# Performance work log

Hardware: AMD Instinct MI355X
Metric: run time of the kernel (lower is better)

## Reference

```python
import jax, jax.numpy as jnp
import numpy as np

B, LQ, LK, LKL = 4, 1024, 1024, 512
DX, H, DK = 1024, 16, 64
ALPHA = 0.5
NEG = -1e9
EPS = 1e-5


def setup_inputs() -> dict:
    key = jax.random.key(0)
    ks = jax.random.split(key, 24)
    s = 0.02
    inp = {
        "q": jax.random.normal(ks[0], (B, LQ, DX), jnp.float32),
        "k": jax.random.normal(ks[1], (B, LK, DX), jnp.float32),
        "v": jax.random.normal(ks[2], (B, LK, DX), jnp.float32),
        "kl": jax.random.normal(ks[3], (B, LKL, DX), jnp.float32),
        "vl": jax.random.normal(ks[4], (B, LKL, DX), jnp.float32),
        "pad_mask": jax.random.randint(ks[5], (B, LQ, LK), 0, 2).astype(bool),
        "pad_mask_l": jax.random.randint(ks[6], (B, LQ, LKL), 0, 2).astype(bool),
        "wq_w": jax.random.normal(ks[7], (DX, H * DK), jnp.float32) * s,
        "wq_b": jnp.zeros((H * DK,), jnp.float32),
        "wk_w": jax.random.normal(ks[8], (DX, H * DK), jnp.float32) * s,
        "wk_b": jnp.zeros((H * DK,), jnp.float32),
        "wv_w": jax.random.normal(ks[9], (DX, H * DK), jnp.float32) * s,
        "wv_b": jnp.zeros((H * DK,), jnp.float32),
        "wkl_w": jax.random.normal(ks[10], (DX, H * DK), jnp.float32) * s,
        "wkl_b": jnp.zeros((H * DK,), jnp.float32),
        "wvl_w": jax.random.normal(ks[11], (DX, H * DK), jnp.float32) * s,
        "wvl_b": jnp.zeros((H * DK,), jnp.float32),
        "wo_w": jax.random.normal(ks[12], (H * DK, DX), jnp.float32) * s,
        "wo_b": jnp.zeros((DX,), jnp.float32),
        "ln_g": jnp.ones((DX,), jnp.float32),
        "ln_b": jnp.zeros((DX,), jnp.float32),
    }
    return inp


def _heads(x, w, b, L):
    # (B, L, DX) @ (DX, H*DK) -> (B, H, L, DK)
    y = x @ w + b
    return y.reshape(B, L, H, DK).transpose(0, 2, 1, 3)


def _attn(qh, kh, vh, mask):
    # qh: (B,H,Lq,D), kh/vh: (B,H,Lk,D), mask: (B,Lq,Lk) bool (True = masked)
    scores = jnp.einsum("bhqd,bhkd->bhqk", qh, kh) / np.sqrt(DK).astype(np.float32)
    scores = jnp.where(mask[:, None, :, :], NEG, scores)
    attn = jax.nn.softmax(scores, axis=-1)
    out = jnp.einsum("bhqk,bhkd->bhqd", attn, vh)
    return out, attn


def reference(q, k, v, kl, vl, pad_mask, pad_mask_l,
              wq_w, wq_b, wk_w, wk_b, wv_w, wv_b,
              wkl_w, wkl_b, wvl_w, wvl_b, wo_w, wo_b, ln_g, ln_b):
    X = q
    qh = _heads(q, wq_w, wq_b, LQ)
    kh = _heads(k, wk_w, wk_b, LK)
    vh = _heads(v, wv_w, wv_b, LK)
    klh = _heads(kl, wkl_w, wkl_b, LKL)
    vlh = _heads(vl, wvl_w, wvl_b, LKL)

    out_c, attn_c = _attn(qh, kh, vh, pad_mask)
    out_l, attn_l = _attn(qh, klh, vlh, pad_mask_l)

    out = ALPHA * out_c + (1.0 - ALPHA) * out_l          # (B,H,Lq,DK)
    out = out.transpose(0, 2, 1, 3).reshape(B, LQ, H * DK)
    out = out @ wo_w + wo_b                              # dropout = identity (eval)
    y = out + X
    mu = jnp.mean(y, axis=-1, keepdims=True)
    var = jnp.var(y, axis=-1, keepdims=True)
    y = (y - mu) / jnp.sqrt(var + EPS) * ln_g + ln_b
    return y, attn_c, attn_l
```

## Files before the change

kernel.cpp:

```cpp
#include <hip/hip_runtime.h>
#include <hip/hip_bf16.h>

#define B_   4
#define LQ_  1024
#define LK_  1024
#define LKL_ 512
#define DX_  1024
#define H_   16
#define DK_  64
#define HDK_ 1024
#define NEG_ -1e9f
#define EPS_ 1e-5f

typedef __bf16 bf16_t;
typedef __bf16 bf16x8 __attribute__((ext_vector_type(8)));
typedef __bf16 bf16x4 __attribute__((ext_vector_type(4)));
typedef float  f32x4  __attribute__((ext_vector_type(4)));

__device__ inline f32x4 mfma16(bf16x8 a, bf16x8 b, f32x4 c) {
    return __builtin_amdgcn_mfma_f32_16x16x32_bf16(a, b, c, 0, 0, 0);
}

__device__ __forceinline__ void gload16(const void* g, void* l) {
    __builtin_amdgcn_global_load_lds(
        (const __attribute__((address_space(1))) void*)g,
        (__attribute__((address_space(3))) void*)l, 16, 0, 0);
}

__device__ inline float waveMax(float v) {
#pragma unroll
    for (int o = 32; o > 0; o >>= 1) v = fmaxf(v, __shfl_xor(v, o, 64));
    return v;
}
__device__ inline float waveSum(float v) {
#pragma unroll
    for (int o = 32; o > 0; o >>= 1) v += __shfl_xor(v, o, 64);
    return v;
}

template<int STRIDE>
__device__ inline int sidx(int row, int col) {
    return (row * STRIDE + col) ^ ((row & 15) << 3);
}

__global__ void detect_mask_kernel(const unsigned* __restrict__ m, unsigned* __restrict__ flag)
{
    __shared__ unsigned w[256];
    w[threadIdx.x] = m[threadIdx.x];
    __syncthreads();
    if (threadIdx.x == 0) {
        bool all01 = true, allf = true;
        for (int i = 0; i < 256; ++i) {
            unsigned v = w[i];
            all01 = all01 && (v <= 1u);
            allf  = allf  && (v == 0u || v == 0x3F800000u);
        }
        *flag = all01 ? 0u : (allf ? 2u : 1u);
    }
}

__global__ __launch_bounds__(256) void bitpack_mask_kernel(
    const void* __restrict__ mc, const void* __restrict__ ml,
    const unsigned* __restrict__ flagp,
    unsigned long long* __restrict__ bc, unsigned long long* __restrict__ bl)
{
    const unsigned flag = *flagp;
    const size_t NC = (size_t)B_ * LQ_ * LK_;
    const int lane = threadIdx.x & 63;
    const size_t g = (size_t)blockIdx.x * 256 + threadIdx.x;
    const bool inC = g < NC;
    const size_t idx = inC ? g : g - NC;
    const void* src = inC ? mc : ml;
    bool m;
    if (flag == 0u)      m = ((const int*)src)[idx] != 0;
    else if (flag == 2u) m = ((const float*)src)[idx] != 0.0f;
    else                 m = ((const unsigned char*)src)[idx] != 0;
    const unsigned long long bal = __ballot(m);
    if (lane == 0) {
        unsigned long long* dst = inC ? bc : bl;
        dst[idx >> 6] = bal;
    }
}

__global__ __launch_bounds__(256) void cvt_bf16_kernel(
    const float* __restrict__ src, bf16_t* __restrict__ dst, int n8)
{
    const int i = blockIdx.x * 256 + threadIdx.x;
    if (i >= n8) return;
    const float4 a = ((const float4*)src)[i * 2];
    const float4 b = ((const float4*)src)[i * 2 + 1];
    bf16x8 o;
    o[0] = (bf16_t)a.x; o[1] = (bf16_t)a.y; o[2] = (bf16_t)a.z; o[3] = (bf16_t)a.w;
    o[4] = (bf16_t)b.x; o[5] = (bf16_t)b.y; o[6] = (bf16_t)b.z; o[7] = (bf16_t)b.w;
    ((bf16x8*)dst)[i] = o;
}

__global__ __launch_bounds__(256) void wtrans_kernel(
    const float* __restrict__ W, bf16_t* __restrict__ Wt)
{
    __shared__ float T[64][65];
    const int k0 = blockIdx.y * 64, n0 = blockIdx.x * 64;
    const int t = threadIdx.x;
    const int lr = t >> 2, c0 = (t & 3) * 16;
#pragma unroll
    for (int j = 0; j < 4; ++j) {
        const float4 v = *(const float4*)&W[(size_t)(k0 + lr) * DX_ + n0 + c0 + j * 4];
        T[lr][c0 + j * 4 + 0] = v.x; T[lr][c0 + j * 4 + 1] = v.y;
        T[lr][c0 + j * 4 + 2] = v.z; T[lr][c0 + j * 4 + 3] = v.w;
    }
    __syncthreads();
    const int dr = t >> 2;
    bf16x8 o0, o1;
#pragma unroll
    for (int j = 0; j < 8; ++j) {
        o0[j] = (bf16_t)T[c0 + j][dr];
        o1[j] = (bf16_t)T[c0 + 8 + j][dr];
    }
    *(bf16x8*)&Wt[(size_t)(n0 + dr) * DX_ + k0 + c0]     = o0;
    *(bf16x8*)&Wt[(size_t)(n0 + dr) * DX_ + k0 + c0 + 8] = o1;
}

__global__ __launch_bounds__(256) void transpose_v_kernel(
    const bf16_t* __restrict__ V, bf16_t* __restrict__ Vt, int L)
{
    __shared__ bf16_t T[64][72];
    const int bh = blockIdx.y, l0 = blockIdx.x * 64;
    const bf16_t* Vb = V + (size_t)bh * L * 64;
    bf16_t* Vtb = Vt + (size_t)bh * 64 * L;
    const int t = threadIdx.x;
    {
        const int lr = t >> 2, dc = (t & 3) * 16;
        const bf16x8 a = *(const bf16x8*)&Vb[(size_t)(l0 + lr) * 64 + dc];
        const bf16x8 b = *(const bf16x8*)&Vb[(size_t)(l0 + lr) * 64 + dc + 8];
#pragma unroll
        for (int j = 0; j < 8; ++j) { T[lr][dc + j] = a[j]; T[lr][dc + 8 + j] = b[j]; }
    }
    __syncthreads();
    {
        const int dr = t >> 2, lc = (t & 3) * 16;
        bf16x8 o0, o1;
#pragma unroll
        for (int j = 0; j < 8; ++j) { o0[j] = T[lc + j][dr]; o1[j] = T[lc + 8 + j][dr]; }
        *(bf16x8*)&Vtb[(size_t)dr * L + l0 + lc]     = o0;
        *(bf16x8*)&Vtb[(size_t)dr * L + l0 + lc + 8] = o1;
    }
}

template<int MODE>
__global__ __launch_bounds__(512, 2) void gemm2_kernel(
    const bf16_t* __restrict__ A, const bf16_t* __restrict__ Bt,
    const float* __restrict__ bias,
    void* __restrict__ out, const float* __restrict__ resid, int lshift)
{
    __shared__ bf16_t As[128 * 64];
    __shared__ bf16_t Bs[128 * 64];
    char* const AsB = (char*)As;
    char* const BsB = (char*)Bs;
    const int tid = threadIdx.x, wave = tid >> 6, lane = tid & 63;
    const int m0 = blockIdx.y * 128, n0 = blockIdx.x * 128;
    const int wr4 = (wave >> 1) * 32, wc2 = (wave & 1) * 64;

    f32x4 acc[2][4] = {};

    const int srow = wave * 8 + (lane >> 3);
    const int sslot = lane & 7;

    for (int k0 = 0; k0 < 1024; k0 += 64) {
        __syncthreads();
#pragma unroll
        for (int j = 0; j < 2; ++j) {
            const int row = srow + j * 64;
            const int gs = sslot ^ (row & 7);
            gload16(&A[(size_t)(m0 + row) * 1024 + k0 + gs * 8],
                    AsB + j * 8192 + wave * 1024);
            gload16(&Bt[(size_t)(n0 + row) * 1024 + k0 + gs * 8],
                    BsB + j * 8192 + wave * 1024);
        }
        __syncthreads();
#pragma unroll
        for (int kk = 0; kk < 2; ++kk) {
            bf16x8 av[2], bv[4];
#pragma unroll
            for (int i = 0; i < 2; ++i) {
                const int r = wr4 + i * 16 + (lane & 15);
                av[i] = *(const bf16x8*)(AsB + r * 128 + (((kk * 4 + (lane >> 4)) ^ (r & 7)) * 16));
            }
#pragma unroll
            for (int n = 0; n < 4; ++n) {
                const int r = wc2 + n * 16 + (lane & 15);
                bv[n] = *(const bf16x8*)(BsB + r * 128 + (((kk * 4 + (lane >> 4)) ^ (r & 7)) * 16));
            }
#pragma unroll
            for (int i = 0; i < 2; ++i)
#pragma unroll
                for (int n = 0; n < 4; ++n)
                    acc[i][n] = mfma16(av[i], bv[n], acc[i][n]);
        }
    }

#pragma unroll
    for (int i = 0; i < 2; ++i) {
#pragma unroll
        for (int n = 0; n < 4; ++n) {
            const int col = n0 + wc2 + n * 16 + (lane & 15);
            const float bs = bias[col];
            const int row0 = m0 + wr4 + i * 16 + (lane >> 4) * 4;
            if (MODE == 0) {
                const int b = row0 >> lshift, l = row0 & ((1 << lshift) - 1);
                const int h = col >> 6, d = col & 63;
#pragma unroll
                for (int r = 0; r < 4; ++r)
                    ((bf16_t*)out)[(((size_t)(b * H_ + h) << lshift) + l + r) * DK_ + d] =
                        (bf16_t)(acc[i][n][r] + bs);
            } else {
#pragma unroll
                for (int r = 0; r < 4; ++r) {
                    const size_t idx = (size_t)(row0 + r) * DX_ + col;
                    ((float*)out)[idx] = acc[i][n][r] + bs + resid[idx];
                }
            }
        }
    }
}

template<int LKX, bool COMBINE>
__device__ __forceinline__ void fused_branch_body(
    const bf16_t* __restrict__ Qh, const bf16_t* __restrict__ Kh,
    const bf16_t* __restrict__ Vt, const unsigned* __restrict__ bits,
    float* __restrict__ S, bf16_t* __restrict__ comb, bf16_t* __restrict__ Ssh)
{
    const int sid = (blockIdx.x & 7) * 512 + (blockIdx.x >> 3);
    const int bh = sid >> 6, qt = sid & 63;
    const int b = bh >> 4, h = bh & 15;
    const int q0 = qt * 16;
    const int wave = threadIdx.x >> 6, lane = threadIdx.x & 63;
    const int lr = lane & 15, lk8 = (lane >> 4) * 8;
    constexpr int WORDS = LKX / 32;

    const bf16_t* Qb  = Qh + (size_t)bh * LQ_ * DK_;
    const bf16_t* Kb  = Kh + (size_t)bh * LKX * DK_;
    const bf16_t* Vtb = Vt + (size_t)bh * DK_ * LKX;
    float* Sout = S + (size_t)bh * LQ_ * LKX;

    bf16x8 qf[2];
#pragma unroll
    for (int ks = 0; ks < 2; ++ks)
        qf[ks] = *(const bf16x8*)&Qb[(size_t)(q0 + lr) * DK_ + ks * 32 + lk8];

    constexpr int KTS = LKX / 64;
#pragma unroll
    for (int kt = 0; kt < KTS; ++kt) {
        const int kbase = wave * (LKX / 4) + kt * 16;
        f32x4 acc = {};
#pragma unroll
        for (int ks = 0; ks < 2; ++ks) {
            const bf16x8 bb = *(const bf16x8*)&Kb[(size_t)(kbase + lr) * DK_ + ks * 32 + lk8];
            acc = mfma16(qf[ks], bb, acc);
        }
        const int wi = kbase >> 5;
        const int sh = (kbase & 16) + (lane & 15);
#pragma unroll
        for (int r = 0; r < 4; ++r) {
            const int row = (lane >> 4) * 4 + r;
            const unsigned word = bits[(size_t)(b * LQ_ + q0 + row) * WORDS + wi];
            const bool msk = (word >> sh) & 1u;
            Ssh[sidx<LKX>(row, kbase + (lane & 15))] = (bf16_t)(msk ? NEG_ : acc[r] * 0.125f);
        }
    }
    __syncthreads();

    constexpr int NP = LKX / 256;
#pragma unroll 1
    for (int i = 0; i < 4; ++i) {
        const int row = wave * 4 + i;
        const int rowg = q0 + row;
        float p[NP * 4];
        float m = -INFINITY;
#pragma unroll
        for (int ps = 0; ps < NP; ++ps) {
            const bf16x4 sv = *(const bf16x4*)&Ssh[sidx<LKX>(row, ps * 256 + lane * 4)];
#pragma unroll
            for (int j = 0; j < 4; ++j) {
                p[ps * 4 + j] = (float)sv[j];
                m = fmaxf(m, p[ps * 4 + j]);
            }
        }
        m = waveMax(m);
        float s = 0.f;
#pragma unroll
        for (int j = 0; j < NP * 4; ++j) { p[j] = __expf(p[j] - m); s += p[j]; }
        s = waveSum(s);
        const float inv = 1.f / s;
#pragma unroll
        for (int ps = 0; ps < NP; ++ps) {
            const int col = ps * 256 + lane * 4;
            f32x4 o; bf16x4 pb;
#pragma unroll
            for (int j = 0; j < 4; ++j) {
                const float v = p[ps * 4 + j] * inv;
                o[j] = v; pb[j] = (bf16_t)v;
            }
            __builtin_nontemporal_store(o, (f32x4*)&Sout[(size_t)rowg * LKX + col]);
            *(bf16x4*)&Ssh[sidx<LKX>(row, col)] = pb;
        }
    }
    __syncthreads();

    f32x4 acc_o = {};
    const int d0 = wave * 16;
#pragma unroll
    for (int ks = 0; ks < LKX / 32; ++ks) {
        const bf16x8 bb = *(const bf16x8*)&Vtb[(size_t)(d0 + lr) * LKX + ks * 32 + lk8];
        const bf16x8 a  = *(const bf16x8*)&Ssh[sidx<LKX>(lr, ks * 32 + lk8)];
        acc_o = mfma16(a, bb, acc_o);
    }

#pragma unroll
    for (int r = 0; r < 4; ++r) {
        const int row = q0 + (lane >> 4) * 4 + r;
        const size_t idx = ((size_t)b * LQ_ + row) * HDK_ + h * DK_ + d0 + (lane & 15);
        const float half = 0.5f * acc_o[r];
        if (COMBINE) comb[idx] = (bf16_t)((float)comb[idx] + half);
        else         comb[idx] = (bf16_t)half;
    }
}

__global__ __launch_bounds__(256, 3) void fused_c_kernel(
    const bf16_t* __restrict__ Qh, const bf16_t* __restrict__ Kh,
    const bf16_t* __restrict__ Vt, const unsigned* __restrict__ bits,
    float* __restrict__ S, bf16_t* __restrict__ comb)
{
    __shared__ bf16_t Ssh[16 * LK_];
    fused_branch_body<LK_, false>(Qh, Kh, Vt, bits, S, comb, Ssh);
}

__global__ __launch_bounds__(256, 3) void fused_l_kernel(
    const bf16_t* __restrict__ Qh, const bf16_t* __restrict__ Kh,
    const bf16_t* __restrict__ Vt, const unsigned* __restrict__ bits,
    float* __restrict__ S, bf16_t* __restrict__ comb)
{
    __shared__ bf16_t Ssh[16 * LKL_];
    fused_branch_body<LKL_, true>(Qh, Kh, Vt, bits, S, comb, Ssh);
}

__global__ __launch_bounds__(256) void ln_kernel(
    const float* __restrict__ Y, const float* __restrict__ g,
    const float* __restrict__ be, float* __restrict__ out)
{
    __shared__ float red1[4], red2[4];
    const int tid = threadIdx.x, wave = tid >> 6, lane = tid & 63;
    const float* p = Y + (size_t)blockIdx.x * DX_;
    const float4 x = *(const float4*)&p[tid * 4];
    float s  = x.x + x.y + x.z + x.w;
    float ss = x.x * x.x + x.y * x.y + x.z * x.z + x.w * x.w;
    s = waveSum(s); ss = waveSum(ss);
    if (lane == 0) { red1[wave] = s; red2[wave] = ss; }
    __syncthreads();
    s  = red1[0] + red1[1] + red1[2] + red1[3];
    ss = red2[0] + red2[1] + red2[2] + red2[3];
    const float mean = s * (1.f / DX_);
    const float var  = ss * (1.f / DX_) - mean * mean;
    const float rstd = rsqrtf(var + EPS_);
    const float4 gg = *(const float4*)&g[tid * 4];
    const float4 bb = *(const float4*)&be[tid * 4];
    float4 o;
    o.x = (x.x - mean) * rstd * gg.x + bb.x;
    o.y = (x.y - mean) * rstd * gg.y + bb.y;
    o.z = (x.z - mean) * rstd * gg.z + bb.z;
    o.w = (x.w - mean) * rstd * gg.w + bb.w;
    *(float4*)&out[(size_t)blockIdx.x * DX_ + tid * 4] = o;
}

extern "C" void kernel_launch(void* const* d_in, const int* in_sizes, int n_in,
                              void* d_out, int out_size, void* d_ws, size_t ws_size,
                              hipStream_t stream)
{
    const float* q    = (const float*)d_in[0];
    const float* k    = (const float*)d_in[1];
    const float* v    = (const float*)d_in[2];
    const float* kl   = (const float*)d_in[3];
    const float* vl   = (const float*)d_in[4];
    const void*  mask  = d_in[5];
    const void*  maskl = d_in[6];
    const float* wq_w  = (const float*)d_in[7];
    const float* wq_b  = (const float*)d_in[8];
    const float* wk_w  = (const float*)d_in[9];
    const float* wk_b  = (const float*)d_in[10];
    const float* wv_w  = (const float*)d_in[11];
    const float* wv_b  = (const float*)d_in[12];
    const float* wkl_w = (const float*)d_in[13];
    const float* wkl_b = (const float*)d_in[14];
    const float* wvl_w = (const float*)d_in[15];
    const float* wvl_b = (const float*)d_in[16];
    const float* wo_w  = (const float*)d_in[17];
    const float* wo_b  = (const float*)d_in[18];
    const float* ln_g  = (const float*)d_in[19];
    const float* ln_b  = (const float*)d_in[20];

    char* ws = (char*)d_ws;
    const size_t MiB = 1u << 20;
    bf16_t* qb   = (bf16_t*)(ws);
    bf16_t* kb   = (bf16_t*)(ws +   8 * MiB);
    bf16_t* vb   = (bf16_t*)(ws +  16 * MiB);
    bf16_t* klb  = (bf16_t*)(ws +  24 * MiB);
    bf16_t* vlb  = (bf16_t*)(ws +  28 * MiB);
    bf16_t* qh   = (bf16_t*)(ws +  32 * MiB);
    bf16_t* kh   = (bf16_t*)(ws +  40 * MiB);
    bf16_t* klh  = (bf16_t*)(ws +  48 * MiB);
    bf16_t* vh   = (bf16_t*)(ws +  52 * MiB);
    bf16_t* vlh  = (bf16_t*)(ws +  60 * MiB);
    bf16_t* vt   = (bf16_t*)(ws +  64 * MiB);
    bf16_t* vlt  = (bf16_t*)(ws +  72 * MiB);
    bf16_t* wqT  = (bf16_t*)(ws +  76 * MiB);
    bf16_t* wkT  = (bf16_t*)(ws +  78 * MiB);
    bf16_t* wvT  = (bf16_t*)(ws +  80 * MiB);
    bf16_t* wklT = (bf16_t*)(ws +  82 * MiB);
    bf16_t* wvlT = (bf16_t*)(ws +  84 * MiB);
    bf16_t* woT  = (bf16_t*)(ws +  86 * MiB);
    unsigned* flag = (unsigned*)(ws + 88 * MiB);
    unsigned long long* bitc = (unsigned long long*)(ws + 89 * MiB);
    unsigned long long* bitl = (unsigned long long*)(ws + 89 * MiB + 512 * 1024);
    bf16_t* comb = (bf16_t*)(ws + 90 * MiB);
    float*  ypre = (float*) (ws);

    float* y_out = (float*)d_out;
    float* Sc = y_out + (size_t)B_ * LQ_ * DX_;
    float* Sl = Sc + (size_t)B_ * H_ * LQ_ * LK_;

    detect_mask_kernel<<<dim3(1), dim3(256), 0, stream>>>((const unsigned*)mask, flag);
    bitpack_mask_kernel<<<dim3((B_*LQ_*(LK_+LKL_)) / 256), 256, 0, stream>>>(
        mask, maskl, flag, bitc, bitl);

    cvt_bf16_kernel<<<2048, 256, 0, stream>>>(q,  qb,  524288);
    cvt_bf16_kernel<<<2048, 256, 0, stream>>>(k,  kb,  524288);
    cvt_bf16_kernel<<<2048, 256, 0, stream>>>(v,  vb,  524288);
    cvt_bf16_kernel<<<1024, 256, 0, stream>>>(kl, klb, 262144);
    cvt_bf16_kernel<<<1024, 256, 0, stream>>>(vl, vlb, 262144);

    wtrans_kernel<<<dim3(16, 16), 256, 0, stream>>>(wq_w,  wqT);
    wtrans_kernel<<<dim3(16, 16), 256, 0, stream>>>(wk_w,  wkT);
    wtrans_kernel<<<dim3(16, 16), 256, 0, stream>>>(wv_w,  wvT);
    wtrans_kernel<<<dim3(16, 16), 256, 0, stream>>>(wkl_w, wklT);
    wtrans_kernel<<<dim3(16, 16), 256, 0, stream>>>(wvl_w, wvlT);
    wtrans_kernel<<<dim3(16, 16), 256, 0, stream>>>(wo_w,  woT);

    gemm2_kernel<0><<<dim3(8, 32), 512, 0, stream>>>(qb,  wqT,  wq_b,  qh,  nullptr, 10);
    gemm2_kernel<0><<<dim3(8, 32), 512, 0, stream>>>(kb,  wkT,  wk_b,  kh,  nullptr, 10);
    gemm2_kernel<0><<<dim3(8, 16), 512, 0, stream>>>(klb, wklT, wkl_b, klh, nullptr,  9);
    gemm2_kernel<0><<<dim3(8, 32), 512, 0, stream>>>(vb,  wvT,  wv_b,  vh,  nullptr, 10);
    gemm2_kernel<0><<<dim3(8, 16), 512, 0, stream>>>(vlb, wvlT, wvl_b, vlh, nullptr,  9);

    transpose_v_kernel<<<dim3(16, 64), 256, 0, stream>>>(vh,  vt,  LK_);
    transpose_v_kernel<<<dim3( 8, 64), 256, 0, stream>>>(vlh, vlt, LKL_);

    fused_c_kernel<<<dim3(4096), 256, 0, stream>>>(qh, kh,  vt,  (const unsigned*)bitc, Sc, comb);
    fused_l_kernel<<<dim3(4096), 256, 0, stream>>>(qh, klh, vlt, (const unsigned*)bitl, Sl, comb);

    gemm2_kernel<2><<<dim3(8, 32), 512, 0, stream>>>(comb, woT, wo_b, ypre, q, 0);

    ln_kernel<<<4096, 256, 0, stream>>>(ypre, ln_g, ln_b, y_out);
}
```

Baseline: 404.7 us.

## Batch prep kernels into grouped launches, add MFMA priority hints, widen softmax vectors

Merges the mask-type detection into the bitpack kernel and collapses the five conversion, six weight-transpose, five projection GEMM and two V-transpose launches into single grouped launches indexed by blockIdx.z. The goal is to cut launch count and the idle gaps between small kernels. Separately, it wraps the MFMA sequences in s_setprio hints, hoists the K loads ahead of the QK MFMAs, and widens the softmax pass to 8-element bf16 vectors. Grouped grids launch some blocks that exit early, and every bitpack block now re-reads the first 256 mask words to detect the mask type.

```diff
diff --git a/kernel.cpp b/kernel.cpp
--- a/kernel.cpp
+++ b/kernel.cpp
@@ -17,6 +17,8 @@
 typedef __bf16 bf16x4 __attribute__((ext_vector_type(4)));
 typedef float  f32x4  __attribute__((ext_vector_type(4)));
 
+typedef __bf16 bf16_t;
+
 __device__ inline f32x4 mfma16(bf16x8 a, bf16x8 b, f32x4 c) {
     return __builtin_amdgcn_mfma_f32_16x16x32_bf16(a, b, c, 0, 0, 0);
 }
@@ -43,28 +45,22 @@
     return (row * STRIDE + col) ^ ((row & 15) << 3);
 }
 
-__global__ void detect_mask_kernel(const unsigned* __restrict__ m, unsigned* __restrict__ flag)
-{
-    __shared__ unsigned w[256];
-    w[threadIdx.x] = m[threadIdx.x];
-    __syncthreads();
-    if (threadIdx.x == 0) {
-        bool all01 = true, allf = true;
-        for (int i = 0; i < 256; ++i) {
-            unsigned v = w[i];
-            all01 = all01 && (v <= 1u);
-            allf  = allf  && (v == 0u || v == 0x3F800000u);
-        }
-        *flag = all01 ? 0u : (allf ? 2u : 1u);
-    }
-}
-
 __global__ __launch_bounds__(256) void bitpack_mask_kernel(
     const void* __restrict__ mc, const void* __restrict__ ml,
-    const unsigned* __restrict__ flagp,
     unsigned long long* __restrict__ bc, unsigned long long* __restrict__ bl)
 {
-    const unsigned flag = *flagp;
+    __shared__ unsigned fl[4];
+    {
+        const unsigned w = ((const unsigned*)mc)[threadIdx.x];
+        const unsigned long long b01 = __ballot(w <= 1u);
+        const unsigned long long bfl = __ballot(w == 0u || w == 0x3F800000u);
+        if ((threadIdx.x & 63) == 0)
+            fl[threadIdx.x >> 6] = ((b01 == ~0ull) ? 1u : 0u) | ((bfl == ~0ull) ? 2u : 0u);
+    }
+    __syncthreads();
+    const unsigned comb = fl[0] & fl[1] & fl[2] & fl[3];
+    const unsigned flag = (comb & 1u) ? 0u : ((comb & 2u) ? 2u : 1u);
+
     const size_t NC = (size_t)B_ * LQ_ * LK_;
     const int lane = threadIdx.x & 63;
     const size_t g = (size_t)blockIdx.x * 256 + threadIdx.x;
@@ -82,23 +78,35 @@
     }
 }
 
-__global__ __launch_bounds__(256) void cvt_bf16_kernel(
-    const float* __restrict__ src, bf16_t* __restrict__ dst, int n8)
-{
+struct CvtArgs {
+    const float* src[5];
+    bf16_t* dst[5];
+    int n8[5];
+};
+__global__ __launch_bounds__(256) void cvt_all_kernel(CvtArgs a)
+{
+    const int z = blockIdx.y;
     const int i = blockIdx.x * 256 + threadIdx.x;
-    if (i >= n8) return;
-    const float4 a = ((const float4*)src)[i * 2];
-    const float4 b = ((const float4*)src)[i * 2 + 1];
+    if (i >= a.n8[z]) return;
+    const float* src = a.src[z];
+    const float4 x = ((const float4*)src)[i * 2];
+    const float4 y = ((const float4*)src)[i * 2 + 1];
     bf16x8 o;
-    o[0] = (bf16_t)a.x; o[1] = (bf16_t)a.y; o[2] = (bf16_t)a.z; o[3] = (bf16_t)a.w;
-    o[4] = (bf16_t)b.x; o[5] = (bf16_t)b.y; o[6] = (bf16_t)b.z; o[7] = (bf16_t)b.w;
-    ((bf16x8*)dst)[i] = o;
-}
-
-__global__ __launch_bounds__(256) void wtrans_kernel(
-    const float* __restrict__ W, bf16_t* __restrict__ Wt)
+    o[0] = (bf16_t)x.x; o[1] = (bf16_t)x.y; o[2] = (bf16_t)x.z; o[3] = (bf16_t)x.w;
+    o[4] = (bf16_t)y.x; o[5] = (bf16_t)y.y; o[6] = (bf16_t)y.z; o[7] = (bf16_t)y.w;
+    ((bf16x8*)a.dst[z])[i] = o;
+}
+
+struct WtArgs {
+    const float* W[6];
+    bf16_t* Wt[6];
+};
+__global__ __launch_bounds__(256) void wtrans_all_kernel(WtArgs a)
 {
     __shared__ float T[64][65];
+    const int z = blockIdx.z;
+    const float* W = a.W[z];
+    bf16_t* Wt = a.Wt[z];
     const int k0 = blockIdx.y * 64, n0 = blockIdx.x * 64;
     const int t = threadIdx.x;
     const int lr = t >> 2, c0 = (t & 3) * 16;
@@ -120,20 +128,28 @@
     *(bf16x8*)&Wt[(size_t)(n0 + dr) * DX_ + k0 + c0 + 8] = o1;
 }
 
-__global__ __launch_bounds__(256) void transpose_v_kernel(
-    const bf16_t* __restrict__ V, bf16_t* __restrict__ Vt, int L)
+struct TvArgs {
+    const bf16_t* V[2];
+    bf16_t* Vt[2];
+    int L[2];
+    int xt[2];
+};
+__global__ __launch_bounds__(256) void transpose_v_all_kernel(TvArgs a)
 {
     __shared__ bf16_t T[64][72];
+    const int z = blockIdx.z;
+    if ((int)blockIdx.x >= a.xt[z]) return;
+    const int L = a.L[z];
     const int bh = blockIdx.y, l0 = blockIdx.x * 64;
-    const bf16_t* Vb = V + (size_t)bh * L * 64;
-    bf16_t* Vtb = Vt + (size_t)bh * 64 * L;
+    const bf16_t* Vb = a.V[z] + (size_t)bh * L * 64;
+    bf16_t* Vtb = a.Vt[z] + (size_t)bh * 64 * L;
     const int t = threadIdx.x;
     {
         const int lr = t >> 2, dc = (t & 3) * 16;
-        const bf16x8 a = *(const bf16x8*)&Vb[(size_t)(l0 + lr) * 64 + dc];
-        const bf16x8 b = *(const bf16x8*)&Vb[(size_t)(l0 + lr) * 64 + dc + 8];
-#pragma unroll
-        for (int j = 0; j < 8; ++j) { T[lr][dc + j] = a[j]; T[lr][dc + 8 + j] = b[j]; }
+        const bf16x8 x = *(const bf16x8*)&Vb[(size_t)(l0 + lr) * 64 + dc];
+        const bf16x8 y = *(const bf16x8*)&Vb[(size_t)(l0 + lr) * 64 + dc + 8];
+#pragma unroll
+        for (int j = 0; j < 8; ++j) { T[lr][dc + j] = x[j]; T[lr][dc + 8 + j] = y[j]; }
     }
     __syncthreads();
     {
@@ -147,13 +163,12 @@
 }
 
 template<int MODE>
-__global__ __launch_bounds__(512, 2) void gemm2_kernel(
+__device__ __forceinline__ void gemm2_body(
     const bf16_t* __restrict__ A, const bf16_t* __restrict__ Bt,
     const float* __restrict__ bias,
-    void* __restrict__ out, const float* __restrict__ resid, int lshift)
-{
-    __shared__ bf16_t As[128 * 64];
-    __shared__ bf16_t Bs[128 * 64];
+    void* __restrict__ out, const float* __restrict__ resid, int lshift,
+    bf16_t* __restrict__ As, bf16_t* __restrict__ Bs)
+{
     char* const AsB = (char*)As;
     char* const BsB = (char*)Bs;
     const int tid = threadIdx.x, wave = tid >> 6, lane = tid & 63;
@@ -190,11 +205,13 @@
                 const int r = wc2 + n * 16 + (lane & 15);
                 bv[n] = *(const bf16x8*)(BsB + r * 128 + (((kk * 4 + (lane >> 4)) ^ (r & 7)) * 16));
             }
+            __builtin_amdgcn_s_setprio(1);
 #pragma unroll
             for (int i = 0; i < 2; ++i)
 #pragma unroll
                 for (int n = 0; n < 4; ++n)
                     acc[i][n] = mfma16(av[i], bv[n], acc[i][n]);
+            __builtin_amdgcn_s_setprio(0);
         }
     }
 
@@ -223,6 +240,33 @@
     }
 }
 
+struct ProjArgs {
+    const bf16_t* A[5];
+    const bf16_t* Bt[5];
+    const float* bias[5];
+    bf16_t* out[5];
+    int mt[5];
+    int lshift[5];
+};
+__global__ __launch_bounds__(512, 2) void proj_gemm_kernel(ProjArgs a)
+{
+    __shared__ bf16_t As[128 * 64];
+    __shared__ bf16_t Bs[128 * 64];
+    const int z = blockIdx.z;
+    if ((int)blockIdx.y >= a.mt[z]) return;
+    gemm2_body<0>(a.A[z], a.Bt[z], a.bias[z], a.out[z], nullptr, a.lshift[z], As, Bs);
+}
+
+__global__ __launch_bounds__(512, 2) void out_gemm_kernel(
+    const bf16_t* __restrict__ A, const bf16_t* __restrict__ Bt,
+    const float* __restrict__ bias, float* __restrict__ out,
+    const float* __restrict__ resid)
+{
+    __shared__ bf16_t As[128 * 64];
+    __shared__ bf16_t Bs[128 * 64];
+    gemm2_body<2>(A, Bt, bias, out, resid, 0, As, Bs);
+}
+
 template<int LKX, bool COMBINE>
 __device__ __forceinline__ void fused_branch_body(
     const bf16_t* __restrict__ Qh, const bf16_t* __restrict__ Kh,
@@ -251,12 +295,13 @@
 #pragma unroll
     for (int kt = 0; kt < KTS; ++kt) {
         const int kbase = wave * (LKX / 4) + kt * 16;
+        const bf16x8 b0 = *(const bf16x8*)&Kb[(size_t)(kbase + lr) * DK_ + lk8];
+        const bf16x8 b1 = *(const bf16x8*)&Kb[(size_t)(kbase + lr) * DK_ + 32 + lk8];
         f32x4 acc = {};
-#pragma unroll
-        for (int ks = 0; ks < 2; ++ks) {
-            const bf16x8 bb = *(const bf16x8*)&Kb[(size_t)(kbase + lr) * DK_ + ks * 32 + lk8];
-            acc = mfma16(qf[ks], bb, acc);
-        }
+        __builtin_amdgcn_s_setprio(1);
+        acc = mfma16(qf[0], b0, acc);
+        acc = mfma16(qf[1], b1, acc);
+        __builtin_amdgcn_s_setprio(0);
         const int wi = kbase >> 5;
         const int sh = (kbase & 16) + (lane & 15);
 #pragma unroll
@@ -269,39 +314,42 @@
     }
     __syncthreads();
 
-    constexpr int NP = LKX / 256;
+    constexpr int NP8 = LKX / 512;
 #pragma unroll 1
     for (int i = 0; i < 4; ++i) {
         const int row = wave * 4 + i;
         const int rowg = q0 + row;
-        float p[NP * 4];
+        float p[NP8 * 8];
         float m = -INFINITY;
 #pragma unroll
-        for (int ps = 0; ps < NP; ++ps) {
-            const bf16x4 sv = *(const bf16x4*)&Ssh[sidx<LKX>(row, ps * 256 + lane * 4)];
-#pragma unroll
-            for (int j = 0; j < 4; ++j) {
-                p[ps * 4 + j] = (float)sv[j];
-                m = fmaxf(m, p[ps * 4 + j]);
+        for (int ps = 0; ps < NP8; ++ps) {
+            const bf16x8 sv = *(const bf16x8*)&Ssh[sidx<LKX>(row, ps * 512 + lane * 8)];
+#pragma unroll
+            for (int j = 0; j < 8; ++j) {
+                p[ps * 8 + j] = (float)sv[j];
+                m = fmaxf(m, p[ps * 8 + j]);
             }
         }
         m = waveMax(m);
         float s = 0.f;
 #pragma unroll
-        for (int j = 0; j < NP * 4; ++j) { p[j] = __expf(p[j] - m); s += p[j]; }
+        for (int j = 0; j < NP8 * 8; ++j) { p[j] = __expf(p[j] - m); s += p[j]; }
         s = waveSum(s);
         const float inv = 1.f / s;
 #pragma unroll
-        for (int ps = 0; ps < NP; ++ps) {
-            const int col = ps * 256 + lane * 4;
-            f32x4 o; bf16x4 pb;
+        for (int ps = 0; ps < NP8; ++ps) {
+            const int col = ps * 512 + lane * 8;
+            f32x4 o0, o1; bf16x8 pb;
 #pragma unroll
             for (int j = 0; j < 4; ++j) {
-                const float v = p[ps * 4 + j] * inv;
-                o[j] = v; pb[j] = (bf16_t)v;
+                const float v0 = p[ps * 8 + j] * inv;
+                const float v1 = p[ps * 8 + 4 + j] * inv;
+                o0[j] = v0; o1[j] = v1;
+                pb[j] = (bf16_t)v0; pb[4 + j] = (bf16_t)v1;
             }
-            __builtin_nontemporal_store(o, (f32x4*)&Sout[(size_t)rowg * LKX + col]);
-            *(bf16x4*)&Ssh[sidx<LKX>(row, col)] = pb;
+            __builtin_nontemporal_store(o0, (f32x4*)&Sout[(size_t)rowg * LKX + col]);
+            __builtin_nontemporal_store(o1, (f32x4*)&Sout[(size_t)rowg * LKX + col + 4]);
+            *(bf16x8*)&Ssh[sidx<LKX>(row, col)] = pb;
         }
     }
     __syncthreads();
@@ -312,7 +360,9 @@
     for (int ks = 0; ks < LKX / 32; ++ks) {
         const bf16x8 bb = *(const bf16x8*)&Vtb[(size_t)(d0 + lr) * LKX + ks * 32 + lk8];
         const bf16x8 a  = *(const bf16x8*)&Ssh[sidx<LKX>(lr, ks * 32 + lk8)];
+        __builtin_amdgcn_s_setprio(1);
         acc_o = mfma16(a, bb, acc_o);
+        __builtin_amdgcn_s_setprio(0);
     }
 
 #pragma unroll
@@ -417,7 +467,6 @@
     bf16_t* wklT = (bf16_t*)(ws +  82 * MiB);
     bf16_t* wvlT = (bf16_t*)(ws +  84 * MiB);
     bf16_t* woT  = (bf16_t*)(ws +  86 * MiB);
-    unsigned* flag = (unsigned*)(ws + 88 * MiB);
     unsigned long long* bitc = (unsigned long long*)(ws + 89 * MiB);
     unsigned long long* bitl = (unsigned long long*)(ws + 89 * MiB + 512 * 1024);
     bf16_t* comb = (bf16_t*)(ws + 90 * MiB);
@@ -427,36 +476,51 @@
     float* Sc = y_out + (size_t)B_ * LQ_ * DX_;
     float* Sl = Sc + (size_t)B_ * H_ * LQ_ * LK_;
 
-    detect_mask_kernel<<<dim3(1), dim3(256), 0, stream>>>((const unsigned*)mask, flag);
     bitpack_mask_kernel<<<dim3((B_*LQ_*(LK_+LKL_)) / 256), 256, 0, stream>>>(
-        mask, maskl, flag, bitc, bitl);
-
-    cvt_bf16_kernel<<<2048, 256, 0, stream>>>(q,  qb,  524288);
-    cvt_bf16_kernel<<<2048, 256, 0, stream>>>(k,  kb,  524288);
-    cvt_bf16_kernel<<<2048, 256, 0, stream>>>(v,  vb,  524288);
-    cvt_bf16_kernel<<<1024, 256, 0, stream>>>(kl, klb, 262144);
-    cvt_bf16_kernel<<<1024, 256, 0, stream>>>(vl, vlb, 262144);
-
-    wtrans_kernel<<<dim3(16, 16), 256, 0, stream>>>(wq_w,  wqT);
-    wtrans_kernel<<<dim3(16, 16), 256, 0, stream>>>(wk_w,  wkT);
-    wtrans_kernel<<<dim3(16, 16), 256, 0, stream>>>(wv_w,  wvT);
-    wtrans_kernel<<<dim3(16, 16), 256, 0, stream>>>(wkl_w, wklT);
-    wtrans_kernel<<<dim3(16, 16), 256, 0, stream>>>(wvl_w, wvlT);
-    wtrans_kernel<<<dim3(16, 16), 256, 0, stream>>>(wo_w,  woT);
-
-    gemm2_kernel<0><<<dim3(8, 32), 512, 0, stream>>>(qb,  wqT,  wq_b,  qh,  nullptr, 10);
-    gemm2_kernel<0><<<dim3(8, 32), 512, 0, stream>>>(kb,  wkT,  wk_b,  kh,  nullptr, 10);
-    gemm2_kernel<0><<<dim3(8, 16), 512, 0, stream>>>(klb, wklT, wkl_b, klh, nullptr,  9);
-    gemm2_kernel<0><<<dim3(8, 32), 512, 0, stream>>>(vb,  wvT,  wv_b,  vh,  nullptr, 10);
-    gemm2_kernel<0><<<dim3(8, 16), 512, 0, stream>>>(vlb, wvlT, wvl_b, vlh, nullptr,  9);
-
-    transpose_v_kernel<<<dim3(16, 64), 256, 0, stream>>>(vh,  vt,  LK_);
-    transpose_v_kernel<<<dim3( 8, 64), 256, 0, stream>>>(vlh, vlt, LKL_);
+        mask, maskl, bitc, bitl);
+
+    {
+        CvtArgs a;
+        a.src[0] = q;  a.dst[0] = qb;  a.n8[0] = 524288;
+        a.src[1] = k;  a.dst[1] = kb;  a.n8[1] = 524288;
+        a.src[2] = v;  a.dst[2] = vb;  a.n8[2] = 524288;
+        a.src[3] = kl; a.dst[3] = klb; a.n8[3] = 262144;
+        a.src[4] = vl; a.dst[4] = vlb; a.n8[4] = 262144;
+        cvt_all_kernel<<<dim3(2048, 5), 256, 0, stream>>>(a);
+    }
+
+    {
+        WtArgs a;
+        a.W[0] = wq_w;  a.Wt[0] = wqT;
+        a.W[1] = wk_w;  a.Wt[1] = wkT;
+        a.W[2] = wv_w;  a.Wt[2] = wvT;
+        a.W[3] = wkl_w; a.Wt[3] = wklT;
+        a.W[4] = wvl_w; a.Wt[4] = wvlT;
+        a.W[5] = wo_w;  a.Wt[5] = woT;
+        wtrans_all_kernel<<<dim3(16, 16, 6), 256, 0, stream>>>(a);
+    }
+
+    {
+        ProjArgs a;
+        a.A[0] = qb;  a.Bt[0] = wqT;  a.bias[0] = wq_b;  a.out[0] = qh;  a.mt[0] = 32; a.lshift[0] = 10;
+        a.A[1] = kb;  a.Bt[1] = wkT;  a.bias[1] = wk_b;  a.out[1] = kh;  a.mt[1] = 32; a.lshift[1] = 10;
+        a.A[2] = klb; a.Bt[2] = wklT; a.bias[2] = wkl_b; a.out[2] = klh; a.mt[2] = 16; a.lshift[2] = 9;
+        a.A[3] = vb;  a.Bt[3] = wvT;  a.bias[3] = wv_b;  a.out[3] = vh;  a.mt[3] = 32; a.lshift[3] = 10;
+        a.A[4] = vlb; a.Bt[4] = wvlT; a.bias[4] = wvl_b; a.out[4] = vlh; a.mt[4] = 16; a.lshift[4] = 9;
+        proj_gemm_kernel<<<dim3(8, 32, 5), 512, 0, stream>>>(a);
+    }
+
+    {
+        TvArgs a;
+        a.V[0] = vh;  a.Vt[0] = vt;  a.L[0] = LK_;  a.xt[0] = 16;
+        a.V[1] = vlh; a.Vt[1] = vlt; a.L[1] = LKL_; a.xt[1] = 8;
+        transpose_v_all_kernel<<<dim3(16, 64, 2), 256, 0, stream>>>(a);
+    }
 
     fused_c_kernel<<<dim3(4096), 256, 0, stream>>>(qh, kh,  vt,  (const unsigned*)bitc, Sc, comb);
     fused_l_kernel<<<dim3(4096), 256, 0, stream>>>(qh, klh, vlt, (const unsigned*)bitl, Sl, comb);
 
-    gemm2_kernel<2><<<dim3(8, 32), 512, 0, stream>>>(comb, woT, wo_b, ypre, q, 0);
+    out_gemm_kernel<<<dim3(8, 32), 512, 0, stream>>>(comb, woT, wo_b, ypre, q);
 
     ln_kernel<<<4096, 256, 0, stream>>>(ypre, ln_g, ln_b, y_out);
 }
```

Result: slower. 417.9 us (+3.3%).
